# Kernel optimization log

Hardware: AMD Instinct MI355X
Metric: run time of the kernel (lower is better)

The kernel has to match this reference:

```python
import jax, jax.numpy as jnp
import numpy as np

H1, H2, F1, F2 = 16, 16, 8, 1

def gcn_conv(x, src, dst, W, b, n_nodes):
    # PyG GCNConv: add self-loops (done by caller), deg-normalized mean-style aggregation
    h = x @ W  # [N, out]
    deg = jax.ops.segment_sum(jnp.ones_like(dst, dtype=h.dtype), dst, num_segments=n_nodes)
    dinv = jnp.where(deg > 0, deg ** -0.5, 0.0)
    norm = dinv[src] * dinv[dst]  # [E]
    agg = jax.ops.segment_sum(h[src] * norm[:, None], dst, num_segments=n_nodes)
    return agg + b


def setup_inputs() -> dict:
    key = jax.random.key(0)
    ks = jax.random.split(key, 12)
    N, E, G, NG = 320000, 5120000, 1000, 32
    x = jax.random.normal(ks[0], (N, 1), dtype=jnp.float32)
    edge_index = jax.random.randint(ks[1], (2, E), 0, N, dtype=jnp.int64)
    y = jax.random.normal(ks[2], (NG * G,), dtype=jnp.float32)
    gene_idx = jax.random.randint(ks[3], (1, G), 0, N // NG, dtype=jnp.int64)
    s = lambda fi, fo: (2.0 / (fi + fo)) ** 0.5
    return {
        'x': x, 'edge_index': edge_index, 'y': y, 'gene_idx': gene_idx, 'num_graphs': NG,
        'W1': jax.random.normal(ks[4], (1, H1), dtype=jnp.float32) * s(1, H1),
        'b1': jnp.zeros((H1,), dtype=jnp.float32),
        'W2': jax.random.normal(ks[5], (H1, H2), dtype=jnp.float32) * s(H1, H2),
        'b2': jnp.zeros((H2,), dtype=jnp.float32),
        'fc1_W': jax.random.normal(ks[6], (H2, F1), dtype=jnp.float32) * s(H2, F1),
        'fc1_b': jnp.zeros((F1,), dtype=jnp.float32),
        'fc2_W': jax.random.normal(ks[7], (F1, F2), dtype=jnp.float32) * s(F1, F2),
        'fc2_b': jnp.zeros((F2,), dtype=jnp.float32),
    }


def reference(x, edge_index, y, gene_idx, num_graphs, W1, b1, W2, b2, fc1_W, fc1_b, fc2_W, fc2_b):
    N = x.shape[0]
    loops = jnp.arange(N, dtype=edge_index.dtype)
    src = jnp.concatenate([edge_index[0], loops])
    dst = jnp.concatenate([edge_index[1], loops])

    h = jax.nn.relu(gcn_conv(x, src, dst, W1, b1, N))
    # F.dropout(p=0.4) is a no-op for a deterministic reference (identity at eval)
    h = jax.nn.relu(gcn_conv(h, src, dst, W2, b2, N))

    # vectorized form of the python gather loop: idx + i * nodes_per_graph, i = 0..reps-1
    nodes_per_graph = N // num_graphs
    reps = y.shape[0] // gene_idx.shape[1]
    offsets = (jnp.arange(reps, dtype=gene_idx.dtype) * nodes_per_graph)[:, None]
    all_idx = (gene_idx[0][None, :] + offsets).reshape(-1)  # [reps*G]
    t = h[all_idx]  # [reps*G, 16]

    t = jax.nn.relu(t @ fc1_W + fc1_b)
    return t @ fc2_W + fc2_b
```

## Files before the change

### kernel.cpp

```cpp
#include <hip/hip_runtime.h>


#define MAXB 17
#define RS_BITS 10
#define RS (1 << RS_BITS)
#define SRC_BITS 19
#define SRC_MASK ((1u << SRC_BITS) - 1u)
#define BT 1024
#define EPT 16
#define TILE (BT * EPT)

__global__ void k_fill_f(float* __restrict__ w, float v, int n) {
    int i = blockIdx.x * blockDim.x + threadIdx.x;
    if (i < n) w[i] = v;
}
__global__ void k_fill_i(int* __restrict__ w, int v, int n) {
    int i = blockIdx.x * blockDim.x + threadIdx.x;
    if (i < n) w[i] = v;
}

__global__ void k_prep(const float* __restrict__ W1, const float* __restrict__ b1,
                       float* __restrict__ bnd, int* __restrict__ prepI) {
    if (threadIdx.x != 0 || blockIdx.x != 0) return;
    float t[16]; int type[16]; int pos[16];
    float thr[16]; int nt = 0;
    for (int j = 0; j < 16; j++) {
        float W = W1[j], B = b1[j];
        if (W > 0.f)      { type[j] = 0; t[j] = -B / W; }
        else if (W < 0.f) { type[j] = 1; t[j] = -B / W; }
        else              { type[j] = (B > 0.f) ? 2 : 3; t[j] = 0.f; }
    }
    for (int j = 0; j < 16; j++) {
        if (type[j] > 1) continue;
        float v = t[j];
        int k = 0; while (k < nt && thr[k] < v) k++;
        if (!(k < nt && thr[k] == v)) {
            for (int m = nt; m > k; m--) thr[m] = thr[m - 1];
            thr[k] = v; nt++;
        }
    }
    int K = nt + 1;
    for (int j = 0; j < 16; j++) {
        if (type[j] <= 1) { int k = 0; while (thr[k] != t[j]) k++; pos[j] = k; }
        else pos[j] = 0;
    }
    for (int k = 0; k < 16; k++) bnd[k] = (k < nt) ? thr[k] : 3.4e38f;
    prepI[0] = K;
    for (int k = 0; k < K; k++) {
        unsigned m = 0;
        for (int j = 0; j < 16; j++) {
            bool act;
            if (type[j] == 0)      act = (k >= pos[j] + 1);
            else if (type[j] == 1) act = (k <= pos[j]);
            else                   act = (type[j] == 2);
            if (act) m |= (1u << j);
        }
        prepI[1 + k] = (int)m;
    }
}

__global__ void k_mark(const int* __restrict__ gene_idx, int* __restrict__ slot,
                       int G, int M, int npg, int N) {
    int i = blockIdx.x * blockDim.x + threadIdx.x;
    if (i >= M) return;
    int node = gene_idx[i % G] + (i / G) * npg;
    if ((unsigned)node < (unsigned)N) slot[node] = i;
}


__global__ void k_hist(const int* __restrict__ dst, int* __restrict__ histG,
                       int E, int N, int R) {
    __shared__ int h[512];
    for (int i = threadIdx.x; i < R; i += blockDim.x) h[i] = 0;
    __syncthreads();
    for (int e = blockIdx.x * blockDim.x + threadIdx.x; e < E; e += gridDim.x * blockDim.x) {
        int d = dst[e];
        if ((unsigned)d < (unsigned)N) atomicAdd(&h[d >> RS_BITS], 1);
    }
    __syncthreads();
    for (int i = threadIdx.x; i < R; i += blockDim.x) {
        int c = h[i];
        if (c) atomicAdd(&histG[i], c);
    }
}

__global__ void k_scan(const int* __restrict__ histG, int* __restrict__ base,
                       int* __restrict__ cursor, int R) {
    __shared__ int a[512];
    int t = threadIdx.x;
    int v = (t < R) ? ((histG[t] + 3) & ~3) : 0;
    a[t] = v;
    __syncthreads();
    for (int off = 1; off < 512; off <<= 1) {
        int add = (t >= off) ? a[t - off] : 0;
        __syncthreads();
        a[t] += add;
        __syncthreads();
    }
    if (t < R) { int ex = a[t] - v; base[t] = ex; cursor[t] = ex; }
}

__global__ void k_bucket(const int* __restrict__ src, const int* __restrict__ dst,
                         int* __restrict__ cursorG, unsigned* __restrict__ bucket,
                         int E, int N, int R, int cap) {
    __shared__ int cnt[512];
    __shared__ int baseL[512];
    int tile0 = blockIdx.x * TILE;
    for (int i = threadIdx.x; i < R; i += BT) cnt[i] = 0;
    __syncthreads();
    int ds[EPT], ss[EPT];
#pragma unroll
    for (int i = 0; i < EPT; i++) {
        int e = tile0 + i * BT + threadIdx.x;
        ds[i] = -1;
        if (e < E) {
            int d = dst[e], s = src[e];
            if ((unsigned)d < (unsigned)N && (unsigned)s < (unsigned)N) {
                ds[i] = d; ss[i] = s;
                atomicAdd(&cnt[d >> RS_BITS], 1);
            }
        }
    }
    __syncthreads();
    for (int r = threadIdx.x; r < R; r += BT) {
        int c = cnt[r];
        baseL[r] = c > 0 ? atomicAdd(&cursorG[r], c) : 0;
        cnt[r] = 0;
    }
    __syncthreads();
#pragma unroll
    for (int i = 0; i < EPT; i++) {
        int d = ds[i];
        if (d < 0) continue;
        int r = d >> RS_BITS;
        int o = atomicAdd(&cnt[r], 1);
        int idx = baseL[r] + o;
        if ((unsigned)idx < (unsigned)cap)
            bucket[idx] = ((unsigned)(d & (RS - 1)) << SRC_BITS) | (unsigned)ss[i];
    }
}

__global__ void __launch_bounds__(BT)
k_degR(const unsigned* __restrict__ bucket, const int* __restrict__ base,
       const int* __restrict__ histG, int* __restrict__ degI, int N, int cap) {
    __shared__ int degL[RS];
    int r = blockIdx.x;
    int nb = base[r];
    int cnt = min(histG[r], cap - nb);
    for (int i = threadIdx.x; i < RS; i += BT) degL[i] = 0;
    __syncthreads();
    for (int i = threadIdx.x * 4; i < cnt; i += BT * 4) {
        uint4 e4 = *(const uint4*)(bucket + nb + i);
        if (i + 0 < cnt) atomicAdd(&degL[e4.x >> SRC_BITS], 1);
        if (i + 1 < cnt) atomicAdd(&degL[e4.y >> SRC_BITS], 1);
        if (i + 2 < cnt) atomicAdd(&degL[e4.z >> SRC_BITS], 1);
        if (i + 3 < cnt) atomicAdd(&degL[e4.w >> SRC_BITS], 1);
    }
    __syncthreads();
    int b0 = r << RS_BITS;
    for (int i = threadIdx.x; i < RS; i += BT) {
        int v = b0 + i;
        if (v < N) degI[v] = degL[i];
    }
}

__global__ void k_dinvp(const int* __restrict__ degI, const float* __restrict__ x,
                        float* __restrict__ sd, float* __restrict__ p, int N) {
    int v = blockIdx.x * blockDim.x + threadIdx.x;
    if (v < N) {
        float di = rsqrtf((float)degI[v] + 1.0f);
        sd[2 * v + 1] = di;
        p[v] = x[v] * di;
    }
}

__global__ void __launch_bounds__(BT)
k_t1R(const unsigned* __restrict__ bucket, const int* __restrict__ base,
      const int* __restrict__ histG, const float* __restrict__ p,
      float* __restrict__ sd, int N, int cap) {
    __shared__ float accL[RS];
    int r = blockIdx.x;
    int nb = base[r];
    int cnt = min(histG[r], cap - nb);
    for (int i = threadIdx.x; i < RS; i += BT) accL[i] = 0.f;
    __syncthreads();
    for (int i = threadIdx.x * 4; i < cnt; i += BT * 4) {
        uint4 e4 = *(const uint4*)(bucket + nb + i);
        if (i + 0 < cnt) atomicAdd(&accL[e4.x >> SRC_BITS], p[e4.x & SRC_MASK]);
        if (i + 1 < cnt) atomicAdd(&accL[e4.y >> SRC_BITS], p[e4.y & SRC_MASK]);
        if (i + 2 < cnt) atomicAdd(&accL[e4.z >> SRC_BITS], p[e4.z & SRC_MASK]);
        if (i + 3 < cnt) atomicAdd(&accL[e4.w >> SRC_BITS], p[e4.w & SRC_MASK]);
    }
    __syncthreads();
    int b0 = r << RS_BITS;
    for (int i = threadIdx.x; i < RS; i += BT) {
        int v = b0 + i;
        if (v < N) sd[2 * v] = accL[i];
    }
}

__global__ void k_s2(const float* __restrict__ p, float* __restrict__ sd, int N) {
    int v = blockIdx.x * blockDim.x + threadIdx.x;
    if (v < N) {
        float di = sd[2 * v + 1];
        sd[2 * v] = di * (sd[2 * v] + p[v]);
    }
}

__global__ void __launch_bounds__(BT)
k_aggR(const unsigned* __restrict__ bucket, const int* __restrict__ base,
       const int* __restrict__ histG, const float* __restrict__ sd,
       const int* __restrict__ slot, const float* __restrict__ bnd,
       const int* __restrict__ prepI, float* __restrict__ aggb, int N, int cap) {
    __shared__ float acc[RS * 8];
    __shared__ int slotL[RS];
    __shared__ float sB[3];
    __shared__ int sK;
    if (threadIdx.x == 0) sK = prepI[0];
    if (threadIdx.x < 3) sB[threadIdx.x] = bnd[threadIdx.x];
    __syncthreads();
    int K = sK;
    if (K > 4) return;
    int r = blockIdx.x;
    int b0 = r << RS_BITS;
    for (int i = threadIdx.x; i < RS; i += BT) {
        int v = b0 + i;
        slotL[i] = (v < N) ? slot[v] : -1;
    }
    for (int i = threadIdx.x; i < RS * 8; i += BT) acc[i] = 0.f;
    __syncthreads();
    int nb = base[r];
    int cnt = min(histG[r], cap - nb);
    const float2* sd2 = (const float2*)sd;
    for (int i = threadIdx.x * 4; i < cnt; i += BT * 4) {
        uint4 e4 = *(const uint4*)(bucket + nb + i);
        unsigned ee[4] = {e4.x, e4.y, e4.z, e4.w};
#pragma unroll
        for (int k4 = 0; k4 < 4; k4++) {
            if (i + k4 >= cnt) break;
            unsigned e = ee[k4];
            int l = (int)(e >> SRC_BITS);
            if (slotL[l] < 0) continue;
            float2 v = sd2[e & SRC_MASK];
            int b = 0;
            for (int k = 0; k < K - 1; k++) b += (v.x > sB[k]) ? 1 : 0;
            atomicAdd(&acc[l * 8 + 2 * b], v.x * v.y);
            atomicAdd(&acc[l * 8 + 2 * b + 1], v.y);
        }
    }
    __syncthreads();
    for (int i = threadIdx.x; i < RS; i += BT) {
        int sl = slotL[i];
        if (sl < 0) continue;
        float* row = aggb + (size_t)sl * (2 * MAXB);
        for (int k = 0; k < K; k++) {
            row[2 * k]     = acc[i * 8 + 2 * k];
            row[2 * k + 1] = acc[i * 8 + 2 * k + 1];
        }
    }
}


__global__ void k_deg(const int* __restrict__ dst, float* __restrict__ deg, int E, int N) {
    int e = blockIdx.x * blockDim.x + threadIdx.x;
    if (e >= E) return;
    int d = dst[e];
    if ((unsigned)d < (unsigned)N) atomicAdd(&deg[d], 1.0f);
}

__global__ void k_dinv_p(const float* __restrict__ x, float* __restrict__ degv,
                         float* __restrict__ p, int N) {
    int v = blockIdx.x * blockDim.x + threadIdx.x;
    if (v < N) {
        float di = rsqrtf(degv[v] + 1.0f);
        degv[v] = di;
        p[v] = x[v] * di;
    }
}

__global__ void k_scatter1(const int* __restrict__ src, const int* __restrict__ dst,
                           const float* __restrict__ p, float* __restrict__ t1, int E, int N) {
    int e = blockIdx.x * blockDim.x + threadIdx.x;
    if (e >= E) return;
    int s = src[e];
    int d = dst[e];
    if ((unsigned)s < (unsigned)N && (unsigned)d < (unsigned)N)
        atomicAdd(&t1[d], p[s]);
}

__global__ void k_s(const float* __restrict__ p, const float* __restrict__ dinv,
                    float* __restrict__ t1, int N) {
    int v = blockIdx.x * blockDim.x + threadIdx.x;
    if (v < N) t1[v] = dinv[v] * (t1[v] + p[v]);
}

__global__ void k_agg_atomic(const int* __restrict__ src, const int* __restrict__ dst,
                             const float* __restrict__ sA, const float* __restrict__ dA,
                             int str, const int* __restrict__ slot,
                             const float* __restrict__ bnd, const int* __restrict__ prepI,
                             float* __restrict__ aggb, int E, int N, int force) {
    __shared__ float sB[16];
    __shared__ int sK;
    if (threadIdx.x == 0) sK = prepI[0];
    if (threadIdx.x < 16) sB[threadIdx.x] = bnd[threadIdx.x];
    __syncthreads();
    int K = sK;
    if (!force && K <= 4) return;
    int T = K - 1;
    for (int e = blockIdx.x * blockDim.x + threadIdx.x; e < E; e += gridDim.x * blockDim.x) {
        int d = dst[e];
        if ((unsigned)d >= (unsigned)N) continue;
        int sl = slot[d];
        if (sl < 0) continue;
        int sv = src[e];
        if ((unsigned)sv >= (unsigned)N) continue;
        float sval = sA[(size_t)sv * str];
        float di = dA[(size_t)sv * str];
        int b = 0;
        for (int i = 0; i < T; i++) b += (sval > sB[i]) ? 1 : 0;
        float* row = aggb + (size_t)sl * (2 * MAXB) + 2 * b;
        atomicAdd(row, sval * di);
        atomicAdd(row + 1, di);
    }
}

__global__ void k_final(const float* __restrict__ aggb, const float* __restrict__ sA,
                        const float* __restrict__ dA, int str,
                        const int* __restrict__ gene_idx, const int* __restrict__ slot,
                        const int* __restrict__ prepI,
                        const float* __restrict__ W1, const float* __restrict__ b1,
                        const float* __restrict__ W2, const float* __restrict__ b2,
                        const float* __restrict__ f1W, const float* __restrict__ f1b,
                        const float* __restrict__ f2W, const float* __restrict__ f2b,
                        float* __restrict__ out, int G, int M, int npg, int N) {
    __shared__ float sW1[16], sb1[16], sW2[256], sb2[16], sf1[128], sf1b[8], sf2[8], sf2b[1];
    __shared__ int sMask[MAXB], sK;
    for (int i = threadIdx.x; i < 256; i += blockDim.x) sW2[i] = W2[i];
    for (int i = threadIdx.x; i < 128; i += blockDim.x) sf1[i] = f1W[i];
    if (threadIdx.x < 16) { sW1[threadIdx.x] = W1[threadIdx.x]; sb1[threadIdx.x] = b1[threadIdx.x]; sb2[threadIdx.x] = b2[threadIdx.x]; }
    if (threadIdx.x < 8)  { sf1b[threadIdx.x] = f1b[threadIdx.x]; sf2[threadIdx.x] = f2W[threadIdx.x]; }
    if (threadIdx.x == 0) { sf2b[0] = f2b[0]; sK = prepI[0]; }
    if (threadIdx.x < MAXB) sMask[threadIdx.x] = prepI[1 + threadIdx.x];
    __syncthreads();

    int i = blockIdx.x * blockDim.x + threadIdx.x;
    if (i >= M) return;
    int node = gene_idx[i % G] + (i / G) * npg;
    if ((unsigned)node >= (unsigned)N) { out[i] = 0.0f; return; }
    int sl = slot[node];

    float di = dA[(size_t)node * str];
    float sval = sA[(size_t)node * str];
    int K = sK;

    float bu[MAXB], bw[MAXB];
    if (sl >= 0) {
        const float* row = aggb + (size_t)sl * (2 * MAXB);
        for (int k = 0; k < K; k++) { bu[k] = row[2 * k]; bw[k] = row[2 * k + 1]; }
    } else {
        for (int k = 0; k < K; k++) { bu[k] = 0.f; bw[k] = 0.f; }
    }

    float a[16];
#pragma unroll
    for (int j = 0; j < 16; j++) {
        float Su = 0.f, Sw = 0.f;
        for (int k = 0; k < K; k++) {
            if ((sMask[k] >> j) & 1) { Su += bu[k]; Sw += bw[k]; }
        }
        float aggj = sW1[j] * Su + sb1[j] * Sw;
        float qself = fmaxf(fmaf(sW1[j], sval, sb1[j]), 0.0f) * di;
        a[j] = di * (aggj + qself);
    }
    float h2[16];
#pragma unroll
    for (int j = 0; j < 16; j++) {
        float acc = sb2[j];
#pragma unroll
        for (int k = 0; k < 16; k++) acc = fmaf(a[k], sW2[k * 16 + j], acc);
        h2[j] = fmaxf(acc, 0.0f);
    }
    float f1[8];
#pragma unroll
    for (int j = 0; j < 8; j++) {
        float acc = sf1b[j];
#pragma unroll
        for (int k = 0; k < 16; k++) acc = fmaf(h2[k], sf1[k * 8 + j], acc);
        f1[j] = fmaxf(acc, 0.0f);
    }
    float o = sf2b[0];
#pragma unroll
    for (int k = 0; k < 8; k++) o = fmaf(f1[k], sf2[k], o);
    out[i] = o;
}

extern "C" void kernel_launch(void* const* d_in, const int* in_sizes, int n_in,
                              void* d_out, int out_size, void* d_ws, size_t ws_size,
                              hipStream_t stream) {
    const float* x        = (const float*)d_in[0];
    const int*   ei       = (const int*)d_in[1];
    const int*   gene_idx = (const int*)d_in[3];
    const float* W1  = (const float*)d_in[5];
    const float* b1  = (const float*)d_in[6];
    const float* W2  = (const float*)d_in[7];
    const float* b2  = (const float*)d_in[8];
    const float* f1W = (const float*)d_in[9];
    const float* f1b = (const float*)d_in[10];
    const float* f2W = (const float*)d_in[11];
    const float* f2b = (const float*)d_in[12];
    float* out = (float*)d_out;

    int N = in_sizes[0];
    int E = in_sizes[1] / 2;
    int M = in_sizes[2];
    int G = in_sizes[3];
    int npg = (int)(((long long)N * (long long)G) / (long long)M);

    const int* src = ei;
    const int* dst = ei + E;

    int R = (N + RS - 1) >> RS_BITS;
    int cap = E + 4 * R + 4;
    const int tb = 256;

    float* ws = (float*)d_ws;
    size_t off = 0;
    float*    sd     = ws + off;              off += (size_t)2 * N;
    int*      slot   = (int*)(ws + off);      off += (size_t)N;
    float*    aggb   = ws + off;
    int*      degI   = (int*)aggb;
    float*    p      = aggb + (size_t)N;      off += (size_t)2 * MAXB * M;
    unsigned* bucket = (unsigned*)(ws + off); off += (size_t)cap;
    int*      histG  = (int*)(ws + off);      off += (size_t)R;
    int*      baseA  = (int*)(ws + off);      off += (size_t)R;
    int*      cursor = (int*)(ws + off);      off += (size_t)R;
    float*    bnd    = ws + off;              off += 16;
    int*      prepI  = (int*)(ws + off);      off += 20;
    size_t need = off * 4;

    bool use_new = (ws_size >= need) && (N < (1 << SRC_BITS)) &&
                   ((size_t)2 * MAXB * M >= (size_t)2 * N) && (R <= 512);

    if (use_new) {
        k_fill_i<<<(N + tb - 1) / tb, tb, 0, stream>>>(slot, -1, N);
        k_fill_i<<<(R + tb - 1) / tb, tb, 0, stream>>>(histG, 0, R);
        k_prep<<<1, 64, 0, stream>>>(W1, b1, bnd, prepI);
        k_mark<<<(M + tb - 1) / tb, tb, 0, stream>>>(gene_idx, slot, G, M, npg, N);
        k_hist<<<512, tb, 0, stream>>>(dst, histG, E, N, R);
        k_scan<<<1, 512, 0, stream>>>(histG, baseA, cursor, R);
        int ntiles = (E + TILE - 1) / TILE;
        k_bucket<<<ntiles, BT, 0, stream>>>(src, dst, cursor, bucket, E, N, R, cap);
        k_degR<<<R, BT, 0, stream>>>(bucket, baseA, histG, degI, N, cap);
        k_dinvp<<<(N + tb - 1) / tb, tb, 0, stream>>>(degI, x, sd, p, N);
        k_t1R<<<R, BT, 0, stream>>>(bucket, baseA, histG, p, sd, N, cap);
        k_s2<<<(N + tb - 1) / tb, tb, 0, stream>>>(p, sd, N);
        k_fill_f<<<(2 * MAXB * M + tb - 1) / tb, tb, 0, stream>>>(aggb, 0.0f, 2 * MAXB * M);
        k_aggR<<<R, BT, 0, stream>>>(bucket, baseA, histG, sd, slot, bnd, prepI, aggb, N, cap);
        k_agg_atomic<<<2048, tb, 0, stream>>>(src, dst, sd, sd + 1, 2, slot, bnd, prepI,
                                              aggb, E, N, 0);
        k_final<<<(M + tb - 1) / tb, tb, 0, stream>>>(aggb, sd, sd + 1, 2, gene_idx, slot,
                                                      prepI, W1, b1, W2, b2, f1W, f1b,
                                                      f2W, f2b, out, G, M, npg, N);
    } else {
        float* deg   = ws;
        float* t1o   = ws + (size_t)N;
        float* pO    = ws + 2 * (size_t)N;
        int*   slotO = (int*)(ws + 3 * (size_t)N);
        float* aggbO = ws + 4 * (size_t)N;
        float* bndO  = aggbO + (size_t)2 * MAXB * M;
        int*   prepO = (int*)(bndO + 16);

        k_fill_f<<<(2 * N + tb - 1) / tb, tb, 0, stream>>>(deg, 0.0f, 2 * N);
        k_fill_i<<<(N + tb - 1) / tb, tb, 0, stream>>>(slotO, -1, N);
        k_fill_f<<<(2 * MAXB * M + tb - 1) / tb, tb, 0, stream>>>(aggbO, 0.0f, 2 * MAXB * M);
        k_prep<<<1, 64, 0, stream>>>(W1, b1, bndO, prepO);
        k_mark<<<(M + tb - 1) / tb, tb, 0, stream>>>(gene_idx, slotO, G, M, npg, N);
        k_deg<<<(E + tb - 1) / tb, tb, 0, stream>>>(dst, deg, E, N);
        k_dinv_p<<<(N + tb - 1) / tb, tb, 0, stream>>>(x, deg, pO, N);
        k_scatter1<<<(E + tb - 1) / tb, tb, 0, stream>>>(src, dst, pO, t1o, E, N);
        k_s<<<(N + tb - 1) / tb, tb, 0, stream>>>(pO, deg, t1o, N);
        k_agg_atomic<<<2048, tb, 0, stream>>>(src, dst, t1o, deg, 1, slotO, bndO, prepO,
                                              aggbO, E, N, 1);
        k_final<<<(M + tb - 1) / tb, tb, 0, stream>>>(aggbO, t1o, deg, 1, gene_idx, slotO,
                                                      prepO, W1, b1, W2, b2, f1W, f1b,
                                                      f2W, f2b, out, G, M, npg, N);
    }
}
```

Before: 270.8 us.

## Split per-range aggregation across sub-blocks with partial buffers and compact slot map

Each destination range's edge list is now split across S sub-blocks, which write partial degree, t1 and aggregation buffers that small merge kernels then reduce. This spreads roughly R blocks' worth of work over R*S blocks to fill the GPU better. Target nodes are compacted per range (up to CMAX), so aggregation shared memory shrinks from RS*8 floats to CMAX*8; nodes beyond that limit fall back to global atomics. The histogram kernel now uses vectorized int4 loads and the bucket kernel uses smaller blocks. The cost is extra kernels, extra partial-buffer traffic and more workspace.

```diff
diff --git a/kernel.cpp b/kernel.cpp
--- a/kernel.cpp
+++ b/kernel.cpp
@@ -6,9 +6,11 @@
 #define RS (1 << RS_BITS)
 #define SRC_BITS 19
 #define SRC_MASK ((1u << SRC_BITS) - 1u)
-#define BT 1024
-#define EPT 16
-#define TILE (BT * EPT)
+#define CMAX 160
+#define PSTRIDE (CMAX * 8)
+#define BK_BT 512
+#define BK_EPT 16
+#define BK_TILE (BK_BT * BK_EPT)
 
 __global__ void k_fill_f(float* __restrict__ w, float v, int n) {
     int i = blockIdx.x * blockDim.x + threadIdx.x;
@@ -67,13 +69,47 @@
     if ((unsigned)node < (unsigned)N) slot[node] = i;
 }
 
+__global__ void k_cmap(int* __restrict__ cm, int* __restrict__ cslot, int* __restrict__ mc,
+                       int N, int R) {
+    __shared__ int cnt;
+    int r = blockIdx.x;
+    if (r >= R) return;
+    if (threadIdx.x == 0) cnt = 0;
+    __syncthreads();
+    int b0 = r << RS_BITS;
+    for (int i = threadIdx.x; i < RS; i += blockDim.x) {
+        int v = b0 + i;
+        if (v >= N) continue;
+        int sl = cm[v];
+        int out;
+        if (sl >= 0) {
+            int c = atomicAdd(&cnt, 1);
+            if (c < CMAX) { cslot[r * CMAX + c] = sl; out = c; }
+            else out = -(sl + 2);
+        } else out = -1;
+        cm[v] = out;
+    }
+    __syncthreads();
+    if (threadIdx.x == 0) mc[r] = min(cnt, CMAX);
+}
+
 
 __global__ void k_hist(const int* __restrict__ dst, int* __restrict__ histG,
                        int E, int N, int R) {
     __shared__ int h[512];
     for (int i = threadIdx.x; i < R; i += blockDim.x) h[i] = 0;
     __syncthreads();
-    for (int e = blockIdx.x * blockDim.x + threadIdx.x; e < E; e += gridDim.x * blockDim.x) {
+    int E4 = E >> 2;
+    const int4* d4 = (const int4*)dst;
+    for (int e = blockIdx.x * blockDim.x + threadIdx.x; e < E4; e += gridDim.x * blockDim.x) {
+        int4 d = d4[e];
+        if ((unsigned)d.x < (unsigned)N) atomicAdd(&h[d.x >> RS_BITS], 1);
+        if ((unsigned)d.y < (unsigned)N) atomicAdd(&h[d.y >> RS_BITS], 1);
+        if ((unsigned)d.z < (unsigned)N) atomicAdd(&h[d.z >> RS_BITS], 1);
+        if ((unsigned)d.w < (unsigned)N) atomicAdd(&h[d.w >> RS_BITS], 1);
+    }
+    for (int e = (E4 << 2) + blockIdx.x * blockDim.x + threadIdx.x; e < E;
+         e += gridDim.x * blockDim.x) {
         int d = dst[e];
         if ((unsigned)d < (unsigned)N) atomicAdd(&h[d >> RS_BITS], 1);
     }
@@ -100,36 +136,42 @@
     if (t < R) { int ex = a[t] - v; base[t] = ex; cursor[t] = ex; }
 }
 
-__global__ void k_bucket(const int* __restrict__ src, const int* __restrict__ dst,
-                         int* __restrict__ cursorG, unsigned* __restrict__ bucket,
-                         int E, int N, int R, int cap) {
+__global__ void __launch_bounds__(BK_BT)
+k_bucket(const int* __restrict__ src, const int* __restrict__ dst,
+         int* __restrict__ cursorG, unsigned* __restrict__ bucket,
+         int E, int N, int R, int cap) {
     __shared__ int cnt[512];
     __shared__ int baseL[512];
-    int tile0 = blockIdx.x * TILE;
-    for (int i = threadIdx.x; i < R; i += BT) cnt[i] = 0;
-    __syncthreads();
-    int ds[EPT], ss[EPT];
-#pragma unroll
-    for (int i = 0; i < EPT; i++) {
-        int e = tile0 + i * BT + threadIdx.x;
-        ds[i] = -1;
-        if (e < E) {
-            int d = dst[e], s = src[e];
-            if ((unsigned)d < (unsigned)N && (unsigned)s < (unsigned)N) {
-                ds[i] = d; ss[i] = s;
-                atomicAdd(&cnt[d >> RS_BITS], 1);
+    int tile0 = blockIdx.x * BK_TILE;
+    for (int i = threadIdx.x; i < R; i += BK_BT) cnt[i] = 0;
+    __syncthreads();
+    int ds[BK_EPT], ss[BK_EPT];
+#pragma unroll
+    for (int c = 0; c < 4; c++) {
+        int e0 = tile0 + c * (BK_BT * 4) + threadIdx.x * 4;
+#pragma unroll
+        for (int k = 0; k < 4; k++) {
+            int e = e0 + k;
+            int idx = c * 4 + k;
+            ds[idx] = -1;
+            if (e < E) {
+                int d = dst[e], s = src[e];
+                if ((unsigned)d < (unsigned)N && (unsigned)s < (unsigned)N) {
+                    ds[idx] = d; ss[idx] = s;
+                    atomicAdd(&cnt[d >> RS_BITS], 1);
+                }
             }
         }
     }
     __syncthreads();
-    for (int r = threadIdx.x; r < R; r += BT) {
+    for (int r = threadIdx.x; r < R; r += BK_BT) {
         int c = cnt[r];
         baseL[r] = c > 0 ? atomicAdd(&cursorG[r], c) : 0;
         cnt[r] = 0;
     }
     __syncthreads();
 #pragma unroll
-    for (int i = 0; i < EPT; i++) {
+    for (int i = 0; i < BK_EPT; i++) {
         int d = ds[i];
         if (d < 0) continue;
         int r = d >> RS_BITS;
@@ -140,80 +182,86 @@
     }
 }
 
-__global__ void __launch_bounds__(BT)
-k_degR(const unsigned* __restrict__ bucket, const int* __restrict__ base,
-       const int* __restrict__ histG, int* __restrict__ degI, int N, int cap) {
+
+__global__ void __launch_bounds__(1024)
+k_degR2(const unsigned* __restrict__ bucket, const int* __restrict__ base,
+        const int* __restrict__ histG, int* __restrict__ pDeg, int cap, int S) {
     __shared__ int degL[RS];
-    int r = blockIdx.x;
+    int r = blockIdx.x / S, q = blockIdx.x % S;
     int nb = base[r];
     int cnt = min(histG[r], cap - nb);
-    for (int i = threadIdx.x; i < RS; i += BT) degL[i] = 0;
-    __syncthreads();
-    for (int i = threadIdx.x * 4; i < cnt; i += BT * 4) {
+    if (cnt < 0) cnt = 0;
+    int lo = (int)(((long long)cnt * q / S) & ~3LL);
+    int hi = (q == S - 1) ? cnt : (int)(((long long)cnt * (q + 1) / S) & ~3LL);
+    for (int i = threadIdx.x; i < RS; i += blockDim.x) degL[i] = 0;
+    __syncthreads();
+    for (int i = lo + threadIdx.x * 4; i < hi; i += blockDim.x * 4) {
         uint4 e4 = *(const uint4*)(bucket + nb + i);
-        if (i + 0 < cnt) atomicAdd(&degL[e4.x >> SRC_BITS], 1);
-        if (i + 1 < cnt) atomicAdd(&degL[e4.y >> SRC_BITS], 1);
-        if (i + 2 < cnt) atomicAdd(&degL[e4.z >> SRC_BITS], 1);
-        if (i + 3 < cnt) atomicAdd(&degL[e4.w >> SRC_BITS], 1);
-    }
-    __syncthreads();
-    int b0 = r << RS_BITS;
-    for (int i = threadIdx.x; i < RS; i += BT) {
-        int v = b0 + i;
-        if (v < N) degI[v] = degL[i];
-    }
-}
-
-__global__ void k_dinvp(const int* __restrict__ degI, const float* __restrict__ x,
-                        float* __restrict__ sd, float* __restrict__ p, int N) {
+        if (i + 0 < hi) atomicAdd(&degL[e4.x >> SRC_BITS], 1);
+        if (i + 1 < hi) atomicAdd(&degL[e4.y >> SRC_BITS], 1);
+        if (i + 2 < hi) atomicAdd(&degL[e4.z >> SRC_BITS], 1);
+        if (i + 3 < hi) atomicAdd(&degL[e4.w >> SRC_BITS], 1);
+    }
+    __syncthreads();
+    int* out = pDeg + (size_t)(r * S + q) * RS;
+    for (int i = threadIdx.x; i < RS; i += blockDim.x) out[i] = degL[i];
+}
+
+__global__ void k_dinvp2(const int* __restrict__ pDeg, const float* __restrict__ x,
+                         float* __restrict__ sd, float* __restrict__ p, int N, int S) {
     int v = blockIdx.x * blockDim.x + threadIdx.x;
-    if (v < N) {
-        float di = rsqrtf((float)degI[v] + 1.0f);
-        sd[2 * v + 1] = di;
-        p[v] = x[v] * di;
-    }
-}
-
-__global__ void __launch_bounds__(BT)
-k_t1R(const unsigned* __restrict__ bucket, const int* __restrict__ base,
-      const int* __restrict__ histG, const float* __restrict__ p,
-      float* __restrict__ sd, int N, int cap) {
+    if (v >= N) return;
+    int r = v >> RS_BITS, l = v & (RS - 1);
+    int deg = 0;
+    for (int q = 0; q < S; q++) deg += pDeg[(size_t)(r * S + q) * RS + l];
+    float di = rsqrtf((float)deg + 1.0f);
+    sd[2 * v + 1] = di;
+    p[v] = x[v] * di;
+}
+
+__global__ void __launch_bounds__(1024)
+k_t1R2(const unsigned* __restrict__ bucket, const int* __restrict__ base,
+       const int* __restrict__ histG, const float* __restrict__ p,
+       float* __restrict__ pT1, int cap, int S) {
     __shared__ float accL[RS];
-    int r = blockIdx.x;
+    int r = blockIdx.x / S, q = blockIdx.x % S;
     int nb = base[r];
     int cnt = min(histG[r], cap - nb);
-    for (int i = threadIdx.x; i < RS; i += BT) accL[i] = 0.f;
-    __syncthreads();
-    for (int i = threadIdx.x * 4; i < cnt; i += BT * 4) {
+    if (cnt < 0) cnt = 0;
+    int lo = (int)(((long long)cnt * q / S) & ~3LL);
+    int hi = (q == S - 1) ? cnt : (int)(((long long)cnt * (q + 1) / S) & ~3LL);
+    for (int i = threadIdx.x; i < RS; i += blockDim.x) accL[i] = 0.f;
+    __syncthreads();
+    for (int i = lo + threadIdx.x * 4; i < hi; i += blockDim.x * 4) {
         uint4 e4 = *(const uint4*)(bucket + nb + i);
-        if (i + 0 < cnt) atomicAdd(&accL[e4.x >> SRC_BITS], p[e4.x & SRC_MASK]);
-        if (i + 1 < cnt) atomicAdd(&accL[e4.y >> SRC_BITS], p[e4.y & SRC_MASK]);
-        if (i + 2 < cnt) atomicAdd(&accL[e4.z >> SRC_BITS], p[e4.z & SRC_MASK]);
-        if (i + 3 < cnt) atomicAdd(&accL[e4.w >> SRC_BITS], p[e4.w & SRC_MASK]);
-    }
-    __syncthreads();
-    int b0 = r << RS_BITS;
-    for (int i = threadIdx.x; i < RS; i += BT) {
-        int v = b0 + i;
-        if (v < N) sd[2 * v] = accL[i];
-    }
-}
-
-__global__ void k_s2(const float* __restrict__ p, float* __restrict__ sd, int N) {
+        if (i + 0 < hi) atomicAdd(&accL[e4.x >> SRC_BITS], p[e4.x & SRC_MASK]);
+        if (i + 1 < hi) atomicAdd(&accL[e4.y >> SRC_BITS], p[e4.y & SRC_MASK]);
+        if (i + 2 < hi) atomicAdd(&accL[e4.z >> SRC_BITS], p[e4.z & SRC_MASK]);
+        if (i + 3 < hi) atomicAdd(&accL[e4.w >> SRC_BITS], p[e4.w & SRC_MASK]);
+    }
+    __syncthreads();
+    float* out = pT1 + (size_t)(r * S + q) * RS;
+    for (int i = threadIdx.x; i < RS; i += blockDim.x) out[i] = accL[i];
+}
+
+__global__ void k_s3(const float* __restrict__ pT1, const float* __restrict__ p,
+                     float* __restrict__ sd, int N, int S) {
     int v = blockIdx.x * blockDim.x + threadIdx.x;
-    if (v < N) {
-        float di = sd[2 * v + 1];
-        sd[2 * v] = di * (sd[2 * v] + p[v]);
-    }
-}
-
-__global__ void __launch_bounds__(BT)
-k_aggR(const unsigned* __restrict__ bucket, const int* __restrict__ base,
+    if (v >= N) return;
+    int r = v >> RS_BITS, l = v & (RS - 1);
+    float t1 = 0.f;
+    for (int q = 0; q < S; q++) t1 += pT1[(size_t)(r * S + q) * RS + l];
+    sd[2 * v] = sd[2 * v + 1] * (t1 + p[v]);
+}
+
+__global__ void __launch_bounds__(1024)
+k_aggS(const unsigned* __restrict__ bucket, const int* __restrict__ base,
        const int* __restrict__ histG, const float* __restrict__ sd,
-       const int* __restrict__ slot, const float* __restrict__ bnd,
-       const int* __restrict__ prepI, float* __restrict__ aggb, int N, int cap) {
-    __shared__ float acc[RS * 8];
-    __shared__ int slotL[RS];
+       const int* __restrict__ cm, const float* __restrict__ bnd,
+       const int* __restrict__ prepI, float* __restrict__ pAgg,
+       float* __restrict__ aggb8, int N, int cap, int S) {
+    __shared__ float acc[PSTRIDE];
+    __shared__ int cmapL[RS];
     __shared__ float sB[3];
     __shared__ int sK;
     if (threadIdx.x == 0) sK = prepI[0];
@@ -221,43 +269,68 @@
     __syncthreads();
     int K = sK;
     if (K > 4) return;
-    int r = blockIdx.x;
+    int r = blockIdx.x / S, q = blockIdx.x % S;
     int b0 = r << RS_BITS;
-    for (int i = threadIdx.x; i < RS; i += BT) {
+    for (int i = threadIdx.x; i < RS; i += blockDim.x) {
         int v = b0 + i;
-        slotL[i] = (v < N) ? slot[v] : -1;
-    }
-    for (int i = threadIdx.x; i < RS * 8; i += BT) acc[i] = 0.f;
+        cmapL[i] = (v < N) ? cm[v] : -1;
+    }
+    for (int i = threadIdx.x; i < PSTRIDE; i += blockDim.x) acc[i] = 0.f;
     __syncthreads();
     int nb = base[r];
     int cnt = min(histG[r], cap - nb);
+    if (cnt < 0) cnt = 0;
+    int lo = (int)(((long long)cnt * q / S) & ~3LL);
+    int hi = (q == S - 1) ? cnt : (int)(((long long)cnt * (q + 1) / S) & ~3LL);
     const float2* sd2 = (const float2*)sd;
-    for (int i = threadIdx.x * 4; i < cnt; i += BT * 4) {
+    for (int i = lo + threadIdx.x * 4; i < hi; i += blockDim.x * 4) {
         uint4 e4 = *(const uint4*)(bucket + nb + i);
         unsigned ee[4] = {e4.x, e4.y, e4.z, e4.w};
 #pragma unroll
         for (int k4 = 0; k4 < 4; k4++) {
-            if (i + k4 >= cnt) break;
+            if (i + k4 >= hi) break;
             unsigned e = ee[k4];
-            int l = (int)(e >> SRC_BITS);
-            if (slotL[l] < 0) continue;
+            int c = cmapL[e >> SRC_BITS];
+            if (c == -1) continue;
             float2 v = sd2[e & SRC_MASK];
             int b = 0;
             for (int k = 0; k < K - 1; k++) b += (v.x > sB[k]) ? 1 : 0;
-            atomicAdd(&acc[l * 8 + 2 * b], v.x * v.y);
-            atomicAdd(&acc[l * 8 + 2 * b + 1], v.y);
+            if (c >= 0) {
+                atomicAdd(&acc[c * 8 + 2 * b], v.x * v.y);
+                atomicAdd(&acc[c * 8 + 2 * b + 1], v.y);
+            } else {
+                int sl = -(c + 2);
+                atomicAdd(&aggb8[(size_t)sl * 8 + 2 * b], v.x * v.y);
+                atomicAdd(&aggb8[(size_t)sl * 8 + 2 * b + 1], v.y);
+            }
         }
     }
     __syncthreads();
-    for (int i = threadIdx.x; i < RS; i += BT) {
-        int sl = slotL[i];
-        if (sl < 0) continue;
-        float* row = aggb + (size_t)sl * (2 * MAXB);
-        for (int k = 0; k < K; k++) {
-            row[2 * k]     = acc[i * 8 + 2 * k];
-            row[2 * k + 1] = acc[i * 8 + 2 * k + 1];
-        }
-    }
+    float* out = pAgg + (size_t)(r * S + q) * PSTRIDE;
+    for (int i = threadIdx.x; i < PSTRIDE; i += blockDim.x) out[i] = acc[i];
+}
+
+__global__ void k_aggMerge(const float* __restrict__ pAgg, const int* __restrict__ cslot,
+                           const int* __restrict__ mc, float* __restrict__ aggb8,
+                           int R, int S) {
+    int idx = blockIdx.x * blockDim.x + threadIdx.x;
+    int per = CMAX * 8;
+    int r = idx / per;
+    if (r >= R) return;
+    int rem = idx % per;
+    int c = rem >> 3, j = rem & 7;
+    if (c >= mc[r]) return;
+    int sl = cslot[r * CMAX + c];
+    if (sl < 0) return;
+    float sum = 0.f;
+    for (int q = 0; q < S; q++) sum += pAgg[(size_t)(r * S + q) * PSTRIDE + c * 8 + j];
+    aggb8[(size_t)sl * 8 + j] = sum;
+}
+
+__global__ void k_fillWide(const int* __restrict__ prepI, float* __restrict__ wide, int n) {
+    if (prepI[0] <= 4) return;
+    int i = blockIdx.x * blockDim.x + threadIdx.x;
+    if (i < n) wide[i] = 0.f;
 }
 
 
@@ -296,9 +369,9 @@
 
 __global__ void k_agg_atomic(const int* __restrict__ src, const int* __restrict__ dst,
                              const float* __restrict__ sA, const float* __restrict__ dA,
-                             int str, const int* __restrict__ slot,
+                             int str, const int* __restrict__ cm, const int* __restrict__ cslot,
                              const float* __restrict__ bnd, const int* __restrict__ prepI,
-                             float* __restrict__ aggb, int E, int N, int force) {
+                             float* __restrict__ wide, int E, int N, int force, int mode) {
     __shared__ float sB[16];
     __shared__ int sK;
     if (threadIdx.x == 0) sK = prepI[0];
@@ -310,7 +383,10 @@
     for (int e = blockIdx.x * blockDim.x + threadIdx.x; e < E; e += gridDim.x * blockDim.x) {
         int d = dst[e];
         if ((unsigned)d >= (unsigned)N) continue;
-        int sl = slot[d];
+        int c = cm[d];
+        int sl;
+        if (mode == 0) sl = c;
+        else sl = (c >= 0) ? cslot[(d >> RS_BITS) * CMAX + c] : (c <= -2 ? -(c + 2) : -1);
         if (sl < 0) continue;
         int sv = src[e];
         if ((unsigned)sv >= (unsigned)N) continue;
@@ -318,21 +394,21 @@
         float di = dA[(size_t)sv * str];
         int b = 0;
         for (int i = 0; i < T; i++) b += (sval > sB[i]) ? 1 : 0;
-        float* row = aggb + (size_t)sl * (2 * MAXB) + 2 * b;
+        float* row = wide + (size_t)sl * (2 * MAXB) + 2 * b;
         atomicAdd(row, sval * di);
         atomicAdd(row + 1, di);
     }
 }
 
-__global__ void k_final(const float* __restrict__ aggb, const float* __restrict__ sA,
-                        const float* __restrict__ dA, int str,
-                        const int* __restrict__ gene_idx, const int* __restrict__ slot,
-                        const int* __restrict__ prepI,
+__global__ void k_final(const float* __restrict__ aggb8, const float* __restrict__ wide,
+                        const float* __restrict__ sA, const float* __restrict__ dA, int str,
+                        const int* __restrict__ gene_idx, const int* __restrict__ cm,
+                        const int* __restrict__ cslot, const int* __restrict__ prepI,
                         const float* __restrict__ W1, const float* __restrict__ b1,
                         const float* __restrict__ W2, const float* __restrict__ b2,
                         const float* __restrict__ f1W, const float* __restrict__ f1b,
                         const float* __restrict__ f2W, const float* __restrict__ f2b,
-                        float* __restrict__ out, int G, int M, int npg, int N) {
+                        float* __restrict__ out, int G, int M, int npg, int N, int mode) {
     __shared__ float sW1[16], sb1[16], sW2[256], sb2[16], sf1[128], sf1b[8], sf2[8], sf2b[1];
     __shared__ int sMask[MAXB], sK;
     for (int i = threadIdx.x; i < 256; i += blockDim.x) sW2[i] = W2[i];
@@ -347,15 +423,19 @@
     if (i >= M) return;
     int node = gene_idx[i % G] + (i / G) * npg;
     if ((unsigned)node >= (unsigned)N) { out[i] = 0.0f; return; }
-    int sl = slot[node];
+    int K = sK;
+    int c = cm[node];
+    int sl;
+    if (mode == 0) sl = c;
+    else sl = (c >= 0) ? cslot[(node >> RS_BITS) * CMAX + c] : (c <= -2 ? -(c + 2) : -1);
 
     float di = dA[(size_t)node * str];
     float sval = sA[(size_t)node * str];
-    int K = sK;
 
     float bu[MAXB], bw[MAXB];
     if (sl >= 0) {
-        const float* row = aggb + (size_t)sl * (2 * MAXB);
+        const float* row = (mode == 1 && K <= 4) ? (aggb8 + (size_t)sl * 8)
+                                                 : (wide + (size_t)sl * (2 * MAXB));
         for (int k = 0; k < K; k++) { bu[k] = row[2 * k]; bw[k] = row[2 * k + 1]; }
     } else {
         for (int k = 0; k < K; k++) { bu[k] = 0.f; bw[k] = 0.f; }
@@ -426,63 +506,80 @@
     float* ws = (float*)d_ws;
     size_t off = 0;
     float*    sd     = ws + off;              off += (size_t)2 * N;
-    int*      slot   = (int*)(ws + off);      off += (size_t)N;
-    float*    aggb   = ws + off;
-    int*      degI   = (int*)aggb;
-    float*    p      = aggb + (size_t)N;      off += (size_t)2 * MAXB * M;
+    int*      cm     = (int*)(ws + off);      off += (size_t)N;
+    float*    p      = ws + off;              off += (size_t)N;
+    float*    aggb8  = ws + off;              off += (size_t)8 * M;
     unsigned* bucket = (unsigned*)(ws + off); off += (size_t)cap;
+    float*    wide   = (float*)bucket;
+    int*      cslot  = (int*)(ws + off);      off += (size_t)R * CMAX;
+    int*      mc     = (int*)(ws + off);      off += (size_t)R;
     int*      histG  = (int*)(ws + off);      off += (size_t)R;
     int*      baseA  = (int*)(ws + off);      off += (size_t)R;
     int*      cursor = (int*)(ws + off);      off += (size_t)R;
     float*    bnd    = ws + off;              off += 16;
     int*      prepI  = (int*)(ws + off);      off += 20;
-    size_t need = off * 4;
-
-    bool use_new = (ws_size >= need) && (N < (1 << SRC_BITS)) &&
-                   ((size_t)2 * MAXB * M >= (size_t)2 * N) && (R <= 512);
+    size_t base_need = off;
+
+    int S = 4;
+    while (S > 1 && (base_need + (size_t)R * S * PSTRIDE) * 4 > ws_size) S >>= 1;
+    float* partial = ws + base_need;
+    int*   partialI = (int*)partial;
+    size_t need = (base_need + (size_t)R * S * PSTRIDE) * 4;
+
+    bool use_new = (need <= ws_size) && (N < (1 << SRC_BITS)) && (R <= 512) &&
+                   ((size_t)cap * 4 >= (size_t)2 * MAXB * M * 4);
 
     if (use_new) {
-        k_fill_i<<<(N + tb - 1) / tb, tb, 0, stream>>>(slot, -1, N);
+        int BTr = (S == 1) ? 1024 : 256;
+        k_fill_i<<<(N + tb - 1) / tb, tb, 0, stream>>>(cm, -1, N);
         k_fill_i<<<(R + tb - 1) / tb, tb, 0, stream>>>(histG, 0, R);
         k_prep<<<1, 64, 0, stream>>>(W1, b1, bnd, prepI);
-        k_mark<<<(M + tb - 1) / tb, tb, 0, stream>>>(gene_idx, slot, G, M, npg, N);
+        k_mark<<<(M + tb - 1) / tb, tb, 0, stream>>>(gene_idx, cm, G, M, npg, N);
+        k_cmap<<<R, tb, 0, stream>>>(cm, cslot, mc, N, R);
         k_hist<<<512, tb, 0, stream>>>(dst, histG, E, N, R);
         k_scan<<<1, 512, 0, stream>>>(histG, baseA, cursor, R);
-        int ntiles = (E + TILE - 1) / TILE;
-        k_bucket<<<ntiles, BT, 0, stream>>>(src, dst, cursor, bucket, E, N, R, cap);
-        k_degR<<<R, BT, 0, stream>>>(bucket, baseA, histG, degI, N, cap);
-        k_dinvp<<<(N + tb - 1) / tb, tb, 0, stream>>>(degI, x, sd, p, N);
-        k_t1R<<<R, BT, 0, stream>>>(bucket, baseA, histG, p, sd, N, cap);
-        k_s2<<<(N + tb - 1) / tb, tb, 0, stream>>>(p, sd, N);
-        k_fill_f<<<(2 * MAXB * M + tb - 1) / tb, tb, 0, stream>>>(aggb, 0.0f, 2 * MAXB * M);
-        k_aggR<<<R, BT, 0, stream>>>(bucket, baseA, histG, sd, slot, bnd, prepI, aggb, N, cap);
-        k_agg_atomic<<<2048, tb, 0, stream>>>(src, dst, sd, sd + 1, 2, slot, bnd, prepI,
-                                              aggb, E, N, 0);
-        k_final<<<(M + tb - 1) / tb, tb, 0, stream>>>(aggb, sd, sd + 1, 2, gene_idx, slot,
-                                                      prepI, W1, b1, W2, b2, f1W, f1b,
-                                                      f2W, f2b, out, G, M, npg, N);
+        int ntiles = (E + BK_TILE - 1) / BK_TILE;
+        k_bucket<<<ntiles, BK_BT, 0, stream>>>(src, dst, cursor, bucket, E, N, R, cap);
+        k_degR2<<<R * S, BTr, 0, stream>>>(bucket, baseA, histG, partialI, cap, S);
+        k_dinvp2<<<(N + tb - 1) / tb, tb, 0, stream>>>(partialI, x, sd, p, N, S);
+        k_t1R2<<<R * S, BTr, 0, stream>>>(bucket, baseA, histG, p, partial, cap, S);
+        k_s3<<<(N + tb - 1) / tb, tb, 0, stream>>>(partial, p, sd, N, S);
+        k_fill_f<<<(8 * M + tb - 1) / tb, tb, 0, stream>>>(aggb8, 0.0f, 8 * M);
+        k_aggS<<<R * S, BTr, 0, stream>>>(bucket, baseA, histG, sd, cm, bnd, prepI,
+                                          partial, aggb8, N, cap, S);
+        k_aggMerge<<<(R * CMAX * 8 + tb - 1) / tb, tb, 0, stream>>>(partial, cslot, mc,
+                                                                    aggb8, R, S);
+        int wn = 2 * MAXB * M;
+        k_fillWide<<<(wn + tb - 1) / tb, tb, 0, stream>>>(prepI, wide, wn);
+        k_agg_atomic<<<2048, tb, 0, stream>>>(src, dst, sd, sd + 1, 2, cm, cslot, bnd,
+                                              prepI, wide, E, N, 0, 1);
+        k_final<<<(M + tb - 1) / tb, tb, 0, stream>>>(aggb8, wide, sd, sd + 1, 2, gene_idx,
+                                                      cm, cslot, prepI, W1, b1, W2, b2,
+                                                      f1W, f1b, f2W, f2b, out, G, M, npg, N,
+                                                      1);
     } else {
         float* deg   = ws;
         float* t1o   = ws + (size_t)N;
         float* pO    = ws + 2 * (size_t)N;
         int*   slotO = (int*)(ws + 3 * (size_t)N);
-        float* aggbO = ws + 4 * (size_t)N;
-        float* bndO  = aggbO + (size_t)2 * MAXB * M;
+        float* wideO = ws + 4 * (size_t)N;
+        float* bndO  = wideO + (size_t)2 * MAXB * M;
         int*   prepO = (int*)(bndO + 16);
 
         k_fill_f<<<(2 * N + tb - 1) / tb, tb, 0, stream>>>(deg, 0.0f, 2 * N);
         k_fill_i<<<(N + tb - 1) / tb, tb, 0, stream>>>(slotO, -1, N);
-        k_fill_f<<<(2 * MAXB * M + tb - 1) / tb, tb, 0, stream>>>(aggbO, 0.0f, 2 * MAXB * M);
+        k_fill_f<<<(2 * MAXB * M + tb - 1) / tb, tb, 0, stream>>>(wideO, 0.0f, 2 * MAXB * M);
         k_prep<<<1, 64, 0, stream>>>(W1, b1, bndO, prepO);
         k_mark<<<(M + tb - 1) / tb, tb, 0, stream>>>(gene_idx, slotO, G, M, npg, N);
         k_deg<<<(E + tb - 1) / tb, tb, 0, stream>>>(dst, deg, E, N);
         k_dinv_p<<<(N + tb - 1) / tb, tb, 0, stream>>>(x, deg, pO, N);
         k_scatter1<<<(E + tb - 1) / tb, tb, 0, stream>>>(src, dst, pO, t1o, E, N);
         k_s<<<(N + tb - 1) / tb, tb, 0, stream>>>(pO, deg, t1o, N);
-        k_agg_atomic<<<2048, tb, 0, stream>>>(src, dst, t1o, deg, 1, slotO, bndO, prepO,
-                                              aggbO, E, N, 1);
-        k_final<<<(M + tb - 1) / tb, tb, 0, stream>>>(aggbO, t1o, deg, 1, gene_idx, slotO,
-                                                      prepO, W1, b1, W2, b2, f1W, f1b,
-                                                      f2W, f2b, out, G, M, npg, N);
-    }
-}
+        k_agg_atomic<<<2048, tb, 0, stream>>>(src, dst, t1o, deg, 1, slotO, (int*)0, bndO,
+                                              prepO, wideO, E, N, 1, 0);
+        k_final<<<(M + tb - 1) / tb, tb, 0, stream>>>((float*)0, wideO, t1o, deg, 1, gene_idx,
+                                                      slotO, (int*)0, prepO, W1, b1, W2, b2,
+                                                      f1W, f1b, f2W, f2b, out, G, M, npg, N,
+                                                      0);
+    }
+}
```

New measurement: 262.8 us. 3.0% less time.
